# Optimization experiments

Hardware: AMD Instinct MI355X
Metric: run time of the kernel (lower is better)

Reference implementation:

```python
import jax, jax.numpy as jnp
import numpy as np

N, IN, HID, OUT, HEADS = 50000, 128, 128, 16, 4
EL, EG = 800000, 200000
NEG_SLOPE = 0.2


def setup_inputs() -> dict:
    key = jax.random.key(0)
    ks = jax.random.split(key, 24)
    def gn(k, shape, fan_in):
        return (jax.random.normal(k, shape, jnp.float32) / np.sqrt(fan_in)).astype(jnp.float32)
    inp = {}
    inp['x'] = jax.random.normal(ks[0], (N, IN), jnp.float32)
    inp['local_edge_index'] = jax.random.randint(ks[1], (2, EL), 0, N, jnp.int64 if jax.config.jax_enable_x64 else jnp.int32)
    inp['global_edge_index'] = jax.random.randint(ks[2], (2, EG), 0, N, jnp.int64 if jax.config.jax_enable_x64 else jnp.int32)
    # local_processor: Linear(IN, HID)
    inp['W1'] = gn(ks[3], (IN, HID), IN); inp['b1'] = jnp.zeros((HID,), jnp.float32)
    # GCNConv(HID, HID): weight + bias
    inp['Wg'] = gn(ks[4], (HID, HID), HID); inp['bg'] = jnp.zeros((HID,), jnp.float32)
    # GATConv(HID, HID, heads=4, concat=False): lin to HEADS*HID, att vectors, bias of size HID
    inp['Wa'] = gn(ks[5], (HID, HEADS * HID), HID)
    inp['att_src'] = gn(ks[6], (HEADS, HID), HID)
    inp['att_dst'] = gn(ks[7], (HEADS, HID), HID)
    inp['ba'] = jnp.zeros((HID,), jnp.float32)
    # hierarchical_pool: Linear(2*HID, HID)
    inp['Wp'] = gn(ks[8], (2 * HID, HID), 2 * HID); inp['bp'] = jnp.zeros((HID,), jnp.float32)
    # classifier: Linear(HID, HID//2) -> ReLU -> Linear(HID//2, OUT)
    inp['Wc1'] = gn(ks[9], (HID, HID // 2), HID); inp['bc1'] = jnp.zeros((HID // 2,), jnp.float32)
    inp['Wc2'] = gn(ks[10], (HID // 2, OUT), HID // 2); inp['bc2'] = jnp.zeros((OUT,), jnp.float32)
    # uncertainty_head: Linear(HID, OUT)
    inp['Wu'] = gn(ks[11], (HID, OUT), HID); inp['bu'] = jnp.zeros((OUT,), jnp.float32)
    return inp


def _add_self_loops(ei, n):
    loop = jnp.arange(n, dtype=ei.dtype)
    return jnp.concatenate([ei[0], loop]), jnp.concatenate([ei[1], loop])


def gcn_conv(x, ei, W, b):
    n = x.shape[0]
    xw = x @ W                                        # [N, HID]
    src, dst = _add_self_loops(ei, n)
    deg = jax.ops.segment_sum(jnp.ones_like(dst, dtype=xw.dtype), dst, num_segments=n)
    dinv = jax.lax.rsqrt(jnp.maximum(deg, 1e-12))     # deg >= 1 thanks to self-loops
    norm = dinv[src] * dinv[dst]                      # [E+N]
    msg = xw[src] * norm[:, None]                     # gather + scale
    return jax.ops.segment_sum(msg, dst, num_segments=n) + b


def gat_conv(x, ei, W, att_src, att_dst, b):
    n = x.shape[0]
    h, c = att_src.shape
    xw = (x @ W).reshape(n, h, c)                     # [N, H, C]
    a_s = jnp.einsum('nhc,hc->nh', xw, att_src)       # [N, H]
    a_d = jnp.einsum('nhc,hc->nh', xw, att_dst)
    src, dst = _add_self_loops(ei, n)
    e = jax.nn.leaky_relu(a_s[src] + a_d[dst], NEG_SLOPE)   # [E+N, H]
    emax = jax.ops.segment_max(e, dst, num_segments=n)      # stable edge-softmax per dst
    ee = jnp.exp(e - emax[dst])
    denom = jax.ops.segment_sum(ee, dst, num_segments=n)
    alpha = ee / (denom[dst] + 1e-16)                        # [E+N, H]
    out = jax.ops.segment_sum(xw[src] * alpha[:, :, None], dst, num_segments=n)  # [N,H,C]
    return out.mean(axis=1) + b                              # concat=False -> head mean


def reference(x, local_edge_index, global_edge_index, W1, b1, Wg, bg, Wa, att_src, att_dst, ba, Wp, bp, Wc1, bc1, Wc2, bc2, Wu, bu):
    x_local = jax.nn.relu(x @ W1 + b1)                       # dropout is identity in eval
    x_lg = jax.nn.relu(gcn_conv(x_local, local_edge_index, Wg, bg))
    x_gg = jax.nn.relu(gat_conv(x_local, global_edge_index, Wa, att_src, att_dst, ba))
    x_comb = jnp.concatenate([x_lg, x_gg], axis=1)           # [N, 2*HID]
    x_pooled = jax.nn.relu(x_comb @ Wp + bp)
    x_final = x_pooled.mean(axis=0, keepdims=True)           # batch=None path
    prediction = jax.nn.relu(x_final @ Wc1 + bc1) @ Wc2 + bc2
    uncertainty = jax.nn.sigmoid(x_final @ Wu + bu)
    return prediction, uncertainty
```

## Files before the change

kernel.cpp:

```cpp
#include <hip/hip_runtime.h>
#include <hip/hip_bf16.h>

#define N_NODES 50000
#define F_IN 128
#define HID 128
#define N_OUT 16
#define HEADS 4
#define EL 800000
#define EG 200000
#define NEG_SLOPE 0.2f
#define NB 196
#define GB 391

typedef short bf16x8 __attribute__((ext_vector_type(8)));
typedef float f32x4 __attribute__((ext_vector_type(4)));
typedef float f32x2 __attribute__((ext_vector_type(2)));

static __device__ __forceinline__ float lrelu(float x) {
    return x > 0.f ? x : NEG_SLOPE * x;
}
static __device__ __forceinline__ unsigned short f2b(float f) {
    __hip_bfloat16 h = __float2bfloat16(f);
    return *reinterpret_cast<unsigned short*>(&h);
}
static __device__ __forceinline__ unsigned char f2fp8(float f) {
    unsigned pk = __builtin_amdgcn_cvt_pk_fp8_f32(f, f, 0, false);
    return (unsigned char)(pk & 0xFF);
}
static __device__ __forceinline__ f32x2 fp8x2_to_f32(unsigned u) {
    return __builtin_amdgcn_cvt_pk_f32_fp8((int)u, false);
}

__global__ __launch_bounds__(256) void conv_hist(
    const float* __restrict__ W1, unsigned short* __restrict__ W1t,
    const float* __restrict__ Wg, unsigned short* __restrict__ Wgt,
    const float* __restrict__ Wa, unsigned short* __restrict__ Wat,
    const float* __restrict__ Wp, unsigned short* __restrict__ Wpt,
    const int* __restrict__ ldst, const int* __restrict__ gdst, int* __restrict__ ghist)
{
    int b = blockIdx.x, t = threadIdx.x;
    if (b < 64) {
        int idx = b * 256 + t;
        int k = idx >> 7, n = idx & 127;
        W1t[n * 128 + k] = f2b(W1[idx]);
    } else if (b < 128) {
        int idx = (b - 64) * 256 + t;
        int k = idx >> 7, n = idx & 127;
        Wgt[n * 128 + k] = f2b(Wg[idx]);
    } else if (b < 384) {
        int idx = (b - 128) * 256 + t;
        int k = idx >> 9, n = idx & 511;
        Wat[(size_t)n * 128 + k] = f2b(Wa[idx]);
    } else if (b < 512) {
        int idx = (b - 384) * 256 + t;
        int k = idx >> 7, n = idx & 127;
        Wpt[(size_t)n * 256 + k] = f2b(Wp[idx]);
    } else {
        __shared__ int lh[NB];
        int blk = b - 512;
        bool loc = blk < 196;
        const int* dstp = loc ? ldst : gdst;
        int nE = loc ? EL : EG;
        int* gh = ghist + (loc ? 0 : NB);
        int start = (loc ? blk : blk - 196) * 4096;
        if (t < NB) lh[t] = 0;
        __syncthreads();
        #pragma unroll
        for (int i = 0; i < 16; i++) {
            int e = start + i * 256 + t;
            if (e < nE) atomicAdd(&lh[dstp[e] >> 8], 1);
        }
        __syncthreads();
        if (t < NB && lh[t]) atomicAdd(&gh[t], lh[t]);
    }
}
__global__ void bucket_scan(const int* __restrict__ ghist,
                            int* __restrict__ bbase, int* __restrict__ gcur)
{
    __shared__ int s[256];
    int g = blockIdx.x, t = threadIdx.x;
    int v = (t < NB) ? ghist[g * NB + t] : 0;
    s[t] = v;
    __syncthreads();
    for (int off = 1; off < 256; off <<= 1) {
        int u = (t >= off) ? s[t - off] : 0;
        __syncthreads();
        s[t] += u;
        __syncthreads();
    }
    if (t < NB) {
        bbase[g * (NB + 1) + t] = s[t] - v;
        gcur[g * NB + t] = s[t] - v;
    }
    if (t == NB - 1) bbase[g * (NB + 1) + NB] = s[t];
}
__global__ __launch_bounds__(256) void bucket_part(
    const int* __restrict__ lsrc, const int* __restrict__ ldst,
    const int* __restrict__ gsrc, const int* __restrict__ gdst,
    int* __restrict__ gcur, unsigned* __restrict__ ebuf_l, unsigned* __restrict__ ebuf_g)
{
    __shared__ int lhist[NB], lbase[NB];
    int blk = blockIdx.x, t = threadIdx.x;
    bool loc = blk < 196;
    const int* srcp = loc ? lsrc : gsrc;
    const int* dstp = loc ? ldst : gdst;
    int nE = loc ? EL : EG;
    unsigned* ebuf = loc ? ebuf_l : ebuf_g;
    int* cur = gcur + (loc ? 0 : NB);
    int start = (loc ? blk : blk - 196) * 4096;
    if (t < NB) lhist[t] = 0;
    __syncthreads();
    unsigned pk[16];
    #pragma unroll
    for (int i = 0; i < 16; i++) {
        int e = start + i * 256 + t;
        if (e < nE) {
            unsigned d = (unsigned)dstp[e];
            pk[i] = (d << 16) | (unsigned)srcp[e];
            atomicAdd(&lhist[d >> 8], 1);
        } else pk[i] = 0xFFFFFFFFu;
    }
    __syncthreads();
    if (t < NB) lbase[t] = atomicAdd(&cur[t], lhist[t]);
    __syncthreads();
    if (t < NB) lhist[t] = 0;
    __syncthreads();
    #pragma unroll
    for (int i = 0; i < 16; i++) {
        unsigned b = pk[i] >> 24;
        if (b < NB) {
            int r = atomicAdd(&lhist[b], 1);
            ebuf[lbase[b] + r] = pk[i];
        }
    }
}
__global__ __launch_bounds__(256) void bucket_csr(
    const unsigned* __restrict__ ebuf_l, const unsigned* __restrict__ ebuf_g,
    const int* __restrict__ bbase,
    int* __restrict__ offs_l, int* __restrict__ offs_g,
    unsigned short* __restrict__ csr_l, unsigned short* __restrict__ csr_g,
    float* __restrict__ dinv)
{
    __shared__ int cnt[256], s[256], cur[256];
    int blk = blockIdx.x, t = threadIdx.x;
    bool loc = blk < 196;
    int b = loc ? blk : blk - 196;
    const unsigned* ebuf = loc ? ebuf_l : ebuf_g;
    const int* bb = bbase + (loc ? 0 : NB + 1);
    int* offs = loc ? offs_l : offs_g;
    unsigned short* csr = loc ? csr_l : csr_g;
    int rs = bb[b], re = bb[b + 1];
    cnt[t] = 0;
    __syncthreads();
    for (int i = rs + t; i < re; i += 256) atomicAdd(&cnt[(ebuf[i] >> 16) & 255], 1);
    __syncthreads();
    int v = cnt[t];
    s[t] = v;
    __syncthreads();
    for (int off = 1; off < 256; off <<= 1) {
        int u = (t >= off) ? s[t - off] : 0;
        __syncthreads();
        s[t] += u;
        __syncthreads();
    }
    int excl = s[t] - v;
    int node = b * 256 + t;
    cur[t] = rs + excl;
    if (node < N_NODES) {
        offs[node] = rs + excl;
        if (loc) dinv[node] = rsqrtf((float)(v + 1));
    }
    if (blk == 0 && t == 0) offs_l[N_NODES] = EL;
    if (blk == 196 && t == 0) offs_g[N_NODES] = EG;
    __syncthreads();
    for (int i = rs + t; i < re; i += 256) {
        unsigned pk = ebuf[i];
        int r = atomicAdd(&cur[(pk >> 16) & 255], 1);
        csr[r] = (unsigned short)(pk & 0xFFFFu);
    }
}

__global__ __launch_bounds__(256) void gemm_x(
    const float* __restrict__ A, const unsigned short* __restrict__ Bt,
    const float* __restrict__ bias, unsigned short* __restrict__ out, int M)
{
    __shared__ unsigned short As[128 * 128];
    __shared__ unsigned short Bs[128 * 128];
    int tid = threadIdx.x;
    int lane = tid & 63, w = tid >> 6;
    int wr = w >> 1, wc = w & 1;
    int l16 = lane & 15, lhi = lane >> 4;
    int m0 = blockIdx.x * 128;
    f32x4 acc[4][4] = {};
    #pragma unroll
    for (int i = 0; i < 8; i++) {
        int u = tid + i * 256;
        int row = u >> 4, e0 = (u & 15) << 3;
        int sw = e0 ^ ((row & 7) << 3);
        int gr = m0 + row;
        unsigned short pb[8] = {};
        if (gr < M) {
            float4 a0 = *(const float4*)(A + (size_t)gr * 128 + e0);
            float4 a1 = *(const float4*)(A + (size_t)gr * 128 + e0 + 4);
            pb[0] = f2b(a0.x); pb[1] = f2b(a0.y); pb[2] = f2b(a0.z); pb[3] = f2b(a0.w);
            pb[4] = f2b(a1.x); pb[5] = f2b(a1.y); pb[6] = f2b(a1.z); pb[7] = f2b(a1.w);
        }
        *(bf16x8*)(As + row * 128 + sw) = *(bf16x8*)pb;
        bf16x8 vb = *(const bf16x8*)(Bt + (size_t)row * 128 + e0);
        *(bf16x8*)(Bs + row * 128 + sw) = vb;
    }
    __syncthreads();
    #pragma unroll
    for (int kk = 0; kk < 4; kk++) {
        int ke = kk * 32 + lhi * 8;
        bf16x8 af[4], bfr[4];
        #pragma unroll
        for (int m = 0; m < 4; m++) {
            int r = wr * 64 + m * 16 + l16;
            af[m] = *(const bf16x8*)(As + r * 128 + (ke ^ ((r & 7) << 3)));
        }
        #pragma unroll
        for (int n = 0; n < 4; n++) {
            int r = wc * 64 + n * 16 + l16;
            bfr[n] = *(const bf16x8*)(Bs + r * 128 + (ke ^ ((r & 7) << 3)));
        }
        #pragma unroll
        for (int m = 0; m < 4; m++)
            #pragma unroll
            for (int n = 0; n < 4; n++)
                acc[m][n] = __builtin_amdgcn_mfma_f32_16x16x32_bf16(af[m], bfr[n], acc[m][n], 0, 0, 0);
    }
    #pragma unroll
    for (int m = 0; m < 4; m++) {
        #pragma unroll
        for (int r = 0; r < 4; r++) {
            int row_g = m0 + wr * 64 + m * 16 + lhi * 4 + r;
            if (row_g >= M) continue;
            #pragma unroll
            for (int n = 0; n < 4; n++) {
                int col_g = wc * 64 + n * 16 + l16;
                float v = fmaxf(acc[m][n][r] + bias[col_g], 0.f);
                out[(size_t)row_g * 128 + col_g] = f2b(v);
            }
        }
    }
}

__global__ __launch_bounds__(256) void gemm_gw(
    const unsigned short* __restrict__ A, const unsigned short* __restrict__ Wgt,
    const unsigned short* __restrict__ Wat,
    unsigned char* __restrict__ xw_g8, unsigned char* __restrict__ xw_a8, int M,
    const float* __restrict__ atts, const float* __restrict__ attd,
    float* __restrict__ a_s, float* __restrict__ a_d)
{
    __shared__ unsigned short As[128 * 128];
    __shared__ unsigned short Bs[128 * 128];
    __shared__ float sas[128], sad[128];
    int tid = threadIdx.x;
    int lane = tid & 63, w = tid >> 6;
    int wr = w >> 1, wc = w & 1;
    int l16 = lane & 15, lhi = lane >> 4;
    int m0 = blockIdx.x * 128;
    int hy = (int)blockIdx.y - 1;
    const unsigned short* Bt = (hy < 0) ? Wgt : (Wat + (size_t)hy * 128 * 128);
    f32x4 acc[4][4] = {};
    #pragma unroll
    for (int i = 0; i < 8; i++) {
        int u = tid + i * 256;
        int row = u >> 4, e0 = (u & 15) << 3;
        int sw = e0 ^ ((row & 7) << 3);
        bf16x8 va = {};
        int gr = m0 + row;
        if (gr < M) va = *(const bf16x8*)(A + (size_t)gr * 128 + e0);
        *(bf16x8*)(As + row * 128 + sw) = va;
        bf16x8 vb = *(const bf16x8*)(Bt + (size_t)row * 128 + e0);
        *(bf16x8*)(Bs + row * 128 + sw) = vb;
    }
    if (tid < 128) { sas[tid] = 0.f; sad[tid] = 0.f; }
    __syncthreads();
    #pragma unroll
    for (int kk = 0; kk < 4; kk++) {
        int ke = kk * 32 + lhi * 8;
        bf16x8 af[4], bfr[4];
        #pragma unroll
        for (int m = 0; m < 4; m++) {
            int r = wr * 64 + m * 16 + l16;
            af[m] = *(const bf16x8*)(As + r * 128 + (ke ^ ((r & 7) << 3)));
        }
        #pragma unroll
        for (int n = 0; n < 4; n++) {
            int r = wc * 64 + n * 16 + l16;
            bfr[n] = *(const bf16x8*)(Bs + r * 128 + (ke ^ ((r & 7) << 3)));
        }
        #pragma unroll
        for (int m = 0; m < 4; m++)
            #pragma unroll
            for (int n = 0; n < 4; n++)
                acc[m][n] = __builtin_amdgcn_mfma_f32_16x16x32_bf16(af[m], bfr[n], acc[m][n], 0, 0, 0);
    }
    if (hy < 0) {
        #pragma unroll
        for (int m = 0; m < 4; m++)
            #pragma unroll
            for (int r = 0; r < 4; r++) {
                int row_g = m0 + wr * 64 + m * 16 + lhi * 4 + r;
                if (row_g >= M) continue;
                #pragma unroll
                for (int n = 0; n < 4; n++) {
                    int col_g = wc * 64 + n * 16 + l16;
                    xw_g8[(size_t)row_g * 128 + col_g] = f2fp8(acc[m][n][r]);
                }
            }
    } else {
        float ats[4], atd[4];
        #pragma unroll
        for (int n = 0; n < 4; n++) {
            int cl = wc * 64 + n * 16 + l16;
            ats[n] = atts[hy * 128 + cl];
            atd[n] = attd[hy * 128 + cl];
        }
        #pragma unroll
        for (int m = 0; m < 4; m++) {
            #pragma unroll
            for (int r = 0; r < 4; r++) {
                int row_l = wr * 64 + m * 16 + lhi * 4 + r;
                int row_g = m0 + row_l;
                float ps = 0.f, pd = 0.f;
                #pragma unroll
                for (int n = 0; n < 4; n++) {
                    float v = acc[m][n][r];
                    ps = fmaf(v, ats[n], ps);
                    pd = fmaf(v, atd[n], pd);
                    if (row_g < M) {
                        int col_g = hy * 128 + wc * 64 + n * 16 + l16;
                        xw_a8[(size_t)row_g * 512 + col_g] = f2fp8(v);
                    }
                }
                #pragma unroll
                for (int off = 1; off < 16; off <<= 1) {
                    ps += __shfl_xor(ps, off);
                    pd += __shfl_xor(pd, off);
                }
                if (l16 == 0) {
                    atomicAdd(&sas[row_l], ps);
                    atomicAdd(&sad[row_l], pd);
                }
            }
        }
        __syncthreads();
        if (tid < 128) {
            int row_g = m0 + tid;
            if (row_g < M) {
                a_s[(size_t)row_g * 4 + hy] = sas[tid];
                a_d[(size_t)row_g * 4 + hy] = sad[tid];
            }
        }
    }
}

__global__ __launch_bounds__(256) void fused_gather(
    const int* __restrict__ offs_l, const unsigned short* __restrict__ csr_l,
    const unsigned char* __restrict__ xw_g8, const float* __restrict__ dinv,
    const float* __restrict__ bg,
    const int* __restrict__ offs_g, const unsigned short* __restrict__ csr_g,
    const float* __restrict__ a_s, const float* __restrict__ a_d,
    const unsigned char* __restrict__ xw_a8, const float* __restrict__ ba,
    unsigned short* __restrict__ xcomb)
{
    int blk = blockIdx.x;
    int lane = threadIdx.x & 63;
    int c2 = lane * 2;
    if (blk < 12500) {
        int d = (blk * 256 + threadIdx.x) >> 6;
        if (d >= N_NODES) return;
        const unsigned short* xg = (const unsigned short*)xw_g8;
        int base = offs_l[d], end = offs_l[d + 1];
        float ax = 0.f, ay = 0.f;
        for (int i = base; i < end; ) {
            int chunk = min(64, end - i);
            int sv = 0; float dvv = 0.f;
            if (lane < chunk) { sv = csr_l[i + lane]; dvv = dinv[sv]; }
            int j = 0;
            for (; j + 8 <= chunk; j += 8) {
                #pragma unroll
                for (int q = 0; q < 8; q++) {
                    int s = __shfl(sv, j + q);
                    float dv = __shfl(dvv, j + q);
                    f32x2 v = fp8x2_to_f32(xg[(size_t)s * 64 + lane]);
                    ax = fmaf(v[0], dv, ax);
                    ay = fmaf(v[1], dv, ay);
                }
            }
            for (; j < chunk; j++) {
                int s = __shfl(sv, j);
                float dv = __shfl(dvv, j);
                f32x2 v = fp8x2_to_f32(xg[(size_t)s * 64 + lane]);
                ax = fmaf(v[0], dv, ax);
                ay = fmaf(v[1], dv, ay);
            }
            i += chunk;
        }
        float dd = dinv[d];
        f32x2 sv2 = fp8x2_to_f32(xg[(size_t)d * 64 + lane]);
        float ox = fmaxf(dd * ax + dd * dd * sv2[0] + bg[c2], 0.f);
        float oy = fmaxf(dd * ay + dd * dd * sv2[1] + bg[c2 + 1], 0.f);
        unsigned uo = (unsigned)f2b(ox) | ((unsigned)f2b(oy) << 16);
        *(unsigned*)(xcomb + (size_t)d * 256 + c2) = uo;
    } else {
        int d = ((blk - 12500) * 256 + threadIdx.x) >> 6;
        if (d >= N_NODES) return;
        const unsigned short* xa = (const unsigned short*)xw_a8;
        int base = offs_g[d], end = offs_g[d + 1];
        int deg = end - base;
        float4 ad4 = *(const float4*)(a_d + (size_t)d * 4);
        float4 asd = *(const float4*)(a_s + (size_t)d * 4);
        float es0 = lrelu(asd.x + ad4.x), es1 = lrelu(asd.y + ad4.y);
        float es2 = lrelu(asd.z + ad4.z), es3 = lrelu(asd.w + ad4.w);
        float ax = 0.f, ay = 0.f;
        float m0, m1, m2, m3, r0, r1, r2, r3;
        if (deg <= 64) {
            int sv = 0;
            float e0 = -1e30f, e1 = -1e30f, e2 = -1e30f, e3 = -1e30f;
            if (lane < deg) {
                sv = csr_g[base + lane];
                float4 s4 = *(const float4*)(a_s + (size_t)sv * 4);
                e0 = lrelu(s4.x + ad4.x); e1 = lrelu(s4.y + ad4.y);
                e2 = lrelu(s4.z + ad4.z); e3 = lrelu(s4.w + ad4.w);
            }
            m0 = e0; m1 = e1; m2 = e2; m3 = e3;
            #pragma unroll
            for (int off = 1; off < 64; off <<= 1) {
                m0 = fmaxf(m0, __shfl_xor(m0, off));
                m1 = fmaxf(m1, __shfl_xor(m1, off));
                m2 = fmaxf(m2, __shfl_xor(m2, off));
                m3 = fmaxf(m3, __shfl_xor(m3, off));
            }
            m0 = fmaxf(m0, es0); m1 = fmaxf(m1, es1);
            m2 = fmaxf(m2, es2); m3 = fmaxf(m3, es3);
            float w0 = (lane < deg) ? __expf(e0 - m0) : 0.f;
            float w1 = (lane < deg) ? __expf(e1 - m1) : 0.f;
            float w2 = (lane < deg) ? __expf(e2 - m2) : 0.f;
            float w3 = (lane < deg) ? __expf(e3 - m3) : 0.f;
            float d0 = w0, d1 = w1, d2 = w2, d3 = w3;
            #pragma unroll
            for (int off = 1; off < 64; off <<= 1) {
                d0 += __shfl_xor(d0, off); d1 += __shfl_xor(d1, off);
                d2 += __shfl_xor(d2, off); d3 += __shfl_xor(d3, off);
            }
            d0 += __expf(es0 - m0); d1 += __expf(es1 - m1);
            d2 += __expf(es2 - m2); d3 += __expf(es3 - m3);
            r0 = 1.f / (d0 + 1e-16f); r1 = 1.f / (d1 + 1e-16f);
            r2 = 1.f / (d2 + 1e-16f); r3 = 1.f / (d3 + 1e-16f);
            for (int j = 0; j < deg; j++) {
                int s = __shfl(sv, j);
                float a0 = __shfl(w0, j) * r0, a1 = __shfl(w1, j) * r1;
                float a2 = __shfl(w2, j) * r2, a3 = __shfl(w3, j) * r3;
                const unsigned short* row = xa + (size_t)s * 256 + lane;
                f32x2 v0 = fp8x2_to_f32(row[0]);
                f32x2 v1 = fp8x2_to_f32(row[64]);
                f32x2 v2 = fp8x2_to_f32(row[128]);
                f32x2 v3 = fp8x2_to_f32(row[192]);
                ax = fmaf(v0[0], a0, ax); ay = fmaf(v0[1], a0, ay);
                ax = fmaf(v1[0], a1, ax); ay = fmaf(v1[1], a1, ay);
                ax = fmaf(v2[0], a2, ax); ay = fmaf(v2[1], a2, ay);
                ax = fmaf(v3[0], a3, ax); ay = fmaf(v3[1], a3, ay);
            }
        } else {
            m0 = es0; m1 = es1; m2 = es2; m3 = es3;
            for (int i = base; i < end; i += 64) {
                int c = min(64, end - i);
                float t0 = -1e30f, t1 = -1e30f, t2 = -1e30f, t3 = -1e30f;
                if (lane < c) {
                    int s = csr_g[i + lane];
                    float4 s4 = *(const float4*)(a_s + (size_t)s * 4);
                    t0 = lrelu(s4.x + ad4.x); t1 = lrelu(s4.y + ad4.y);
                    t2 = lrelu(s4.z + ad4.z); t3 = lrelu(s4.w + ad4.w);
                }
                m0 = fmaxf(m0, t0); m1 = fmaxf(m1, t1);
                m2 = fmaxf(m2, t2); m3 = fmaxf(m3, t3);
            }
            #pragma unroll
            for (int off = 1; off < 64; off <<= 1) {
                m0 = fmaxf(m0, __shfl_xor(m0, off));
                m1 = fmaxf(m1, __shfl_xor(m1, off));
                m2 = fmaxf(m2, __shfl_xor(m2, off));
                m3 = fmaxf(m3, __shfl_xor(m3, off));
            }
            float d0 = 0.f, d1 = 0.f, d2 = 0.f, d3 = 0.f;
            for (int i = base; i < end; i += 64) {
                int c = min(64, end - i);
                if (lane < c) {
                    int s = csr_g[i + lane];
                    float4 s4 = *(const float4*)(a_s + (size_t)s * 4);
                    d0 += __expf(lrelu(s4.x + ad4.x) - m0);
                    d1 += __expf(lrelu(s4.y + ad4.y) - m1);
                    d2 += __expf(lrelu(s4.z + ad4.z) - m2);
                    d3 += __expf(lrelu(s4.w + ad4.w) - m3);
                }
            }
            #pragma unroll
            for (int off = 1; off < 64; off <<= 1) {
                d0 += __shfl_xor(d0, off); d1 += __shfl_xor(d1, off);
                d2 += __shfl_xor(d2, off); d3 += __shfl_xor(d3, off);
            }
            d0 += __expf(es0 - m0); d1 += __expf(es1 - m1);
            d2 += __expf(es2 - m2); d3 += __expf(es3 - m3);
            r0 = 1.f / (d0 + 1e-16f); r1 = 1.f / (d1 + 1e-16f);
            r2 = 1.f / (d2 + 1e-16f); r3 = 1.f / (d3 + 1e-16f);
            for (int i = base; i < end; i += 64) {
                int c = min(64, end - i);
                int sv = 0;
                float w0 = 0.f, w1 = 0.f, w2 = 0.f, w3 = 0.f;
                if (lane < c) {
                    sv = csr_g[i + lane];
                    float4 s4 = *(const float4*)(a_s + (size_t)sv * 4);
                    w0 = __expf(lrelu(s4.x + ad4.x) - m0) * r0;
                    w1 = __expf(lrelu(s4.y + ad4.y) - m1) * r1;
                    w2 = __expf(lrelu(s4.z + ad4.z) - m2) * r2;
                    w3 = __expf(lrelu(s4.w + ad4.w) - m3) * r3;
                }
                for (int j = 0; j < c; j++) {
                    int s = __shfl(sv, j);
                    float a0 = __shfl(w0, j), a1 = __shfl(w1, j);
                    float a2 = __shfl(w2, j), a3 = __shfl(w3, j);
                    const unsigned short* row = xa + (size_t)s * 256 + lane;
                    f32x2 v0 = fp8x2_to_f32(row[0]);
                    f32x2 v1 = fp8x2_to_f32(row[64]);
                    f32x2 v2 = fp8x2_to_f32(row[128]);
                    f32x2 v3 = fp8x2_to_f32(row[192]);
                    ax = fmaf(v0[0], a0, ax); ay = fmaf(v0[1], a0, ay);
                    ax = fmaf(v1[0], a1, ax); ay = fmaf(v1[1], a1, ay);
                    ax = fmaf(v2[0], a2, ax); ay = fmaf(v2[1], a2, ay);
                    ax = fmaf(v3[0], a3, ax); ay = fmaf(v3[1], a3, ay);
                }
            }
        }
        float s0 = __expf(es0 - m0) * r0, s1 = __expf(es1 - m1) * r1;
        float s2 = __expf(es2 - m2) * r2, s3 = __expf(es3 - m3) * r3;
        const unsigned short* row = xa + (size_t)d * 256 + lane;
        f32x2 v0 = fp8x2_to_f32(row[0]);
        f32x2 v1 = fp8x2_to_f32(row[64]);
        f32x2 v2 = fp8x2_to_f32(row[128]);
        f32x2 v3 = fp8x2_to_f32(row[192]);
        ax = fmaf(v0[0], s0, ax); ay = fmaf(v0[1], s0, ay);
        ax = fmaf(v1[0], s1, ax); ay = fmaf(v1[1], s1, ay);
        ax = fmaf(v2[0], s2, ax); ay = fmaf(v2[1], s2, ay);
        ax = fmaf(v3[0], s3, ax); ay = fmaf(v3[1], s3, ay);
        float ox = fmaxf(0.25f * ax + ba[c2], 0.f);
        float oy = fmaxf(0.25f * ay + ba[c2 + 1], 0.f);
        unsigned uo = (unsigned)f2b(ox) | ((unsigned)f2b(oy) << 16);
        *(unsigned*)(xcomb + (size_t)d * 256 + 128 + c2) = uo;
    }
}

__global__ __launch_bounds__(256) void mfma_pool(
    const unsigned short* __restrict__ A, const unsigned short* __restrict__ Bt,
    const float* __restrict__ bp, float* __restrict__ sumvec, int M)
{
    __shared__ unsigned short As[128 * 128];
    __shared__ unsigned short Bs[128 * 128];
    __shared__ float red[128];
    int tid = threadIdx.x;
    int lane = tid & 63, w = tid >> 6;
    int wr = w >> 1, wc = w & 1;
    int l16 = lane & 15, lhi = lane >> 4;
    int m0 = blockIdx.x * 128;
    f32x4 acc[4][4] = {};
    for (int kb = 0; kb < 256; kb += 128) {
        if (kb) __syncthreads();
        #pragma unroll
        for (int i = 0; i < 8; i++) {
            int u = tid + i * 256;
            int row = u >> 4, e0 = (u & 15) << 3;
            int sw = e0 ^ ((row & 7) << 3);
            bf16x8 va = {};
            int gr = m0 + row;
            if (gr < M) va = *(const bf16x8*)(A + (size_t)gr * 256 + kb + e0);
            *(bf16x8*)(As + row * 128 + sw) = va;
            bf16x8 vb = *(const bf16x8*)(Bt + (size_t)row * 256 + kb + e0);
            *(bf16x8*)(Bs + row * 128 + sw) = vb;
        }
        __syncthreads();
        #pragma unroll
        for (int kk = 0; kk < 4; kk++) {
            int ke = kk * 32 + lhi * 8;
            bf16x8 af[4], bfr[4];
            #pragma unroll
            for (int m = 0; m < 4; m++) {
                int r = wr * 64 + m * 16 + l16;
                af[m] = *(const bf16x8*)(As + r * 128 + (ke ^ ((r & 7) << 3)));
            }
            #pragma unroll
            for (int n = 0; n < 4; n++) {
                int r = wc * 64 + n * 16 + l16;
                bfr[n] = *(const bf16x8*)(Bs + r * 128 + (ke ^ ((r & 7) << 3)));
            }
            #pragma unroll
            for (int m = 0; m < 4; m++)
                #pragma unroll
                for (int n = 0; n < 4; n++)
                    acc[m][n] = __builtin_amdgcn_mfma_f32_16x16x32_bf16(af[m], bfr[n], acc[m][n], 0, 0, 0);
        }
    }
    float bcol[4];
    #pragma unroll
    for (int n = 0; n < 4; n++) bcol[n] = bp[wc * 64 + n * 16 + l16];
    float colsum[4] = {0.f, 0.f, 0.f, 0.f};
    #pragma unroll
    for (int m = 0; m < 4; m++) {
        #pragma unroll
        for (int r = 0; r < 4; r++) {
            int row_g = m0 + wr * 64 + m * 16 + lhi * 4 + r;
            if (row_g < M) {
                #pragma unroll
                for (int n = 0; n < 4; n++)
                    colsum[n] += fmaxf(acc[m][n][r] + bcol[n], 0.f);
            }
        }
    }
    #pragma unroll
    for (int n = 0; n < 4; n++) {
        colsum[n] += __shfl_xor(colsum[n], 16);
        colsum[n] += __shfl_xor(colsum[n], 32);
    }
    if (tid < 128) red[tid] = 0.f;
    __syncthreads();
    if (lhi == 0) {
        #pragma unroll
        for (int n = 0; n < 4; n++)
            atomicAdd(&red[wc * 64 + n * 16 + l16], colsum[n]);
    }
    __syncthreads();
    if (tid < 128) atomicAdd(&sumvec[tid], red[tid]);
}

__global__ void final_head(const float* __restrict__ sumvec,
                           const float* __restrict__ Wc1, const float* __restrict__ bc1,
                           const float* __restrict__ Wc2, const float* __restrict__ bc2,
                           const float* __restrict__ Wu, const float* __restrict__ bu,
                           float* __restrict__ out)
{
    __shared__ float xf[128];
    __shared__ float h1[64];
    int t = threadIdx.x;
    xf[t] = sumvec[t] * (1.0f / N_NODES);
    __syncthreads();
    if (t < 64) {
        float s = bc1[t];
        for (int c = 0; c < 128; c++) s = fmaf(xf[c], Wc1[c * 64 + t], s);
        h1[t] = fmaxf(s, 0.f);
    }
    __syncthreads();
    if (t < 16) {
        float s = bc2[t];
        for (int j = 0; j < 64; j++) s = fmaf(h1[j], Wc2[j * 16 + t], s);
        out[t] = s;
        float u = bu[t];
        for (int c = 0; c < 128; c++) u = fmaf(xf[c], Wu[c * 16 + t], u);
        out[16 + t] = 1.0f / (1.0f + expf(-u));
    }
}

extern "C" void kernel_launch(void* const* d_in, const int* in_sizes, int n_in,
                              void* d_out, int out_size, void* d_ws, size_t ws_size,
                              hipStream_t stream) {
    const float* x    = (const float*)d_in[0];
    const int*   lei  = (const int*)d_in[1];
    const int*   gei  = (const int*)d_in[2];
    const float* W1   = (const float*)d_in[3];
    const float* b1   = (const float*)d_in[4];
    const float* Wg   = (const float*)d_in[5];
    const float* bg   = (const float*)d_in[6];
    const float* Wa   = (const float*)d_in[7];
    const float* atts = (const float*)d_in[8];
    const float* attd = (const float*)d_in[9];
    const float* ba   = (const float*)d_in[10];
    const float* Wp   = (const float*)d_in[11];
    const float* bp   = (const float*)d_in[12];
    const float* Wc1  = (const float*)d_in[13];
    const float* bc1  = (const float*)d_in[14];
    const float* Wc2  = (const float*)d_in[15];
    const float* bc2  = (const float*)d_in[16];
    const float* Wu   = (const float*)d_in[17];
    const float* bu   = (const float*)d_in[18];

    const int* lsrc = lei;
    const int* ldst = lei + EL;
    const int* gsrc = gei;
    const int* gdst = gei + EG;

    uintptr_t base = (uintptr_t)d_ws;
    auto alloc = [&](size_t bytes) { void* p = (void*)base; base += (bytes + 255) & ~(size_t)255; return p; };
    unsigned short* x_loc  = (unsigned short*)alloc((size_t)N_NODES * 128 * 2);
    unsigned char*  xw_g8  = (unsigned char*)alloc((size_t)N_NODES * 128);
    unsigned char*  xw_a8  = (unsigned char*)alloc((size_t)N_NODES * 512);
    unsigned short* xcomb  = (unsigned short*)alloc((size_t)N_NODES * 256 * 2);
    unsigned short* W1t    = (unsigned short*)alloc((size_t)128 * 128 * 2);
    unsigned short* Wgt    = (unsigned short*)alloc((size_t)128 * 128 * 2);
    unsigned short* Wat    = (unsigned short*)alloc((size_t)512 * 128 * 2);
    unsigned short* Wpt    = (unsigned short*)alloc((size_t)128 * 256 * 2);
    float* dinv       = (float*)alloc((size_t)N_NODES * 4);
    float* a_s        = (float*)alloc((size_t)N_NODES * 4 * 4);
    float* a_d        = (float*)alloc((size_t)N_NODES * 4 * 4);
    int*   ghist      = (int*)alloc((size_t)2 * NB * 4);
    int*   bbase      = (int*)alloc((size_t)2 * (NB + 1) * 4);
    int*   gcur       = (int*)alloc((size_t)2 * NB * 4);
    unsigned* ebuf_l  = (unsigned*)alloc((size_t)EL * 4);
    unsigned* ebuf_g  = (unsigned*)alloc((size_t)EG * 4);
    int*   offs_l     = (int*)alloc(((size_t)N_NODES + 1) * 4);
    int*   offs_g     = (int*)alloc(((size_t)N_NODES + 1) * 4);
    unsigned short* csr_l = (unsigned short*)alloc((size_t)EL * 2);
    unsigned short* csr_g = (unsigned short*)alloc((size_t)EG * 2);
    float* sumvec     = (float*)alloc(128 * 4);

    hipMemsetAsync(ghist, 0, (size_t)2 * NB * 4, stream);
    hipMemsetAsync(sumvec, 0, 128 * 4, stream);

    conv_hist<<<757, 256, 0, stream>>>(W1, W1t, Wg, Wgt, Wa, Wat, Wp, Wpt,
                                       ldst, gdst, ghist);
    bucket_scan<<<2, 256, 0, stream>>>(ghist, bbase, gcur);
    bucket_part<<<245, 256, 0, stream>>>(lsrc, ldst, gsrc, gdst, gcur, ebuf_l, ebuf_g);
    bucket_csr<<<392, 256, 0, stream>>>(ebuf_l, ebuf_g, bbase, offs_l, offs_g,
                                        csr_l, csr_g, dinv);

    gemm_x<<<GB, 256, 0, stream>>>(x, W1t, b1, x_loc, N_NODES);

    gemm_gw<<<dim3(GB, 5), 256, 0, stream>>>(x_loc, Wgt, Wat, xw_g8, xw_a8, N_NODES,
                                             atts, attd, a_s, a_d);

    fused_gather<<<25000, 256, 0, stream>>>(offs_l, csr_l, xw_g8, dinv, bg,
                                            offs_g, csr_g, a_s, a_d, xw_a8, ba, xcomb);

    mfma_pool<<<GB, 256, 0, stream>>>(xcomb, Wpt, bp, sumvec, N_NODES);
    final_head<<<1, 128, 0, stream>>>(sumvec, Wc1, bc1, Wc2, bc2, Wu, bu,
                                      (float*)d_out);
}
```

Before: 193.6 us.

## Restructure gather to wide 8-byte loads with sub-wave edge parallelism

The GCN gather now splits each wavefront into four 16-lane groups. Each group handles a different edge and loads 8 fp8 values per lane, and the groups' partial sums are combined with cross-group shuffles at the end. The GAT small-degree path maps each 16-lane group to one head, broadcasts source indices and weights with readlane, and applies the softmax normalization once per edge. The aim is fewer, wider memory transactions and fewer shuffle instructions per edge, at the cost of extra reduction shuffles and idle lanes during the final store.

```diff
diff --git a/kernel.cpp b/kernel.cpp
--- a/kernel.cpp
+++ b/kernel.cpp
@@ -29,6 +29,9 @@
 }
 static __device__ __forceinline__ f32x2 fp8x2_to_f32(unsigned u) {
     return __builtin_amdgcn_cvt_pk_f32_fp8((int)u, false);
+}
+static __device__ __forceinline__ float rdlane_f(float v, int l) {
+    return __int_as_float(__builtin_amdgcn_readlane(__float_as_int(v), l));
 }
 
 __global__ __launch_bounds__(256) void conv_hist(
@@ -369,55 +372,69 @@
 {
     int blk = blockIdx.x;
     int lane = threadIdx.x & 63;
-    int c2 = lane * 2;
+    int g = lane >> 4, q = lane & 15;
     if (blk < 12500) {
         int d = (blk * 256 + threadIdx.x) >> 6;
         if (d >= N_NODES) return;
-        const unsigned short* xg = (const unsigned short*)xw_g8;
         int base = offs_l[d], end = offs_l[d + 1];
-        float ax = 0.f, ay = 0.f;
+        float acc[8] = {};
         for (int i = base; i < end; ) {
             int chunk = min(64, end - i);
             int sv = 0; float dvv = 0.f;
             if (lane < chunk) { sv = csr_l[i + lane]; dvv = dinv[sv]; }
-            int j = 0;
-            for (; j + 8 <= chunk; j += 8) {
-                #pragma unroll
-                for (int q = 0; q < 8; q++) {
-                    int s = __shfl(sv, j + q);
-                    float dv = __shfl(dvv, j + q);
-                    f32x2 v = fp8x2_to_f32(xg[(size_t)s * 64 + lane]);
-                    ax = fmaf(v[0], dv, ax);
-                    ay = fmaf(v[1], dv, ay);
-                }
-            }
-            for (; j < chunk; j++) {
-                int s = __shfl(sv, j);
-                float dv = __shfl(dvv, j);
-                f32x2 v = fp8x2_to_f32(xg[(size_t)s * 64 + lane]);
-                ax = fmaf(v[0], dv, ax);
-                ay = fmaf(v[1], dv, ay);
+            int nst = (chunk + 3) >> 2;
+            for (int j = 0; j < nst; j++) {
+                int e = j * 4 + g;
+                int s = __shfl(sv, e);
+                float dv = __shfl(dvv, e);
+                if (e >= chunk) dv = 0.f;
+                uint2 v = *(const uint2*)(xw_g8 + (size_t)s * 128 + q * 8);
+                f32x2 p0 = __builtin_amdgcn_cvt_pk_f32_fp8((int)v.x, false);
+                f32x2 p1 = __builtin_amdgcn_cvt_pk_f32_fp8((int)v.x, true);
+                f32x2 p2 = __builtin_amdgcn_cvt_pk_f32_fp8((int)v.y, false);
+                f32x2 p3 = __builtin_amdgcn_cvt_pk_f32_fp8((int)v.y, true);
+                acc[0] = fmaf(p0[0], dv, acc[0]); acc[1] = fmaf(p0[1], dv, acc[1]);
+                acc[2] = fmaf(p1[0], dv, acc[2]); acc[3] = fmaf(p1[1], dv, acc[3]);
+                acc[4] = fmaf(p2[0], dv, acc[4]); acc[5] = fmaf(p2[1], dv, acc[5]);
+                acc[6] = fmaf(p3[0], dv, acc[6]); acc[7] = fmaf(p3[1], dv, acc[7]);
             }
             i += chunk;
         }
-        float dd = dinv[d];
-        f32x2 sv2 = fp8x2_to_f32(xg[(size_t)d * 64 + lane]);
-        float ox = fmaxf(dd * ax + dd * dd * sv2[0] + bg[c2], 0.f);
-        float oy = fmaxf(dd * ay + dd * dd * sv2[1] + bg[c2 + 1], 0.f);
-        unsigned uo = (unsigned)f2b(ox) | ((unsigned)f2b(oy) << 16);
-        *(unsigned*)(xcomb + (size_t)d * 256 + c2) = uo;
+        #pragma unroll
+        for (int k = 0; k < 8; k++) {
+            acc[k] += __shfl_xor(acc[k], 16);
+            acc[k] += __shfl_xor(acc[k], 32);
+        }
+        if (g == 0) {
+            float dd = dinv[d];
+            float d2 = dd * dd;
+            uint2 sv2 = *(const uint2*)(xw_g8 + (size_t)d * 128 + q * 8);
+            f32x2 s0 = __builtin_amdgcn_cvt_pk_f32_fp8((int)sv2.x, false);
+            f32x2 s1 = __builtin_amdgcn_cvt_pk_f32_fp8((int)sv2.x, true);
+            f32x2 s2 = __builtin_amdgcn_cvt_pk_f32_fp8((int)sv2.y, false);
+            f32x2 s3 = __builtin_amdgcn_cvt_pk_f32_fp8((int)sv2.y, true);
+            float sf[8] = {s0[0], s0[1], s1[0], s1[1], s2[0], s2[1], s3[0], s3[1]};
+            float4 b0 = *(const float4*)(bg + q * 8);
+            float4 b1 = *(const float4*)(bg + q * 8 + 4);
+            float bb[8] = {b0.x, b0.y, b0.z, b0.w, b1.x, b1.y, b1.z, b1.w};
+            unsigned o[4];
+            #pragma unroll
+            for (int k = 0; k < 4; k++) {
+                float v0 = fmaxf(dd * acc[2 * k] + d2 * sf[2 * k] + bb[2 * k], 0.f);
+                float v1 = fmaxf(dd * acc[2 * k + 1] + d2 * sf[2 * k + 1] + bb[2 * k + 1], 0.f);
+                o[k] = (unsigned)f2b(v0) | ((unsigned)f2b(v1) << 16);
+            }
+            *(uint4*)(xcomb + (size_t)d * 256 + q * 8) = make_uint4(o[0], o[1], o[2], o[3]);
+        }
     } else {
         int d = ((blk - 12500) * 256 + threadIdx.x) >> 6;
         if (d >= N_NODES) return;
-        const unsigned short* xa = (const unsigned short*)xw_a8;
         int base = offs_g[d], end = offs_g[d + 1];
         int deg = end - base;
         float4 ad4 = *(const float4*)(a_d + (size_t)d * 4);
         float4 asd = *(const float4*)(a_s + (size_t)d * 4);
         float es0 = lrelu(asd.x + ad4.x), es1 = lrelu(asd.y + ad4.y);
         float es2 = lrelu(asd.z + ad4.z), es3 = lrelu(asd.w + ad4.w);
-        float ax = 0.f, ay = 0.f;
-        float m0, m1, m2, m3, r0, r1, r2, r3;
         if (deg <= 64) {
             int sv = 0;
             float e0 = -1e30f, e1 = -1e30f, e2 = -1e30f, e3 = -1e30f;
@@ -427,7 +444,7 @@
                 e0 = lrelu(s4.x + ad4.x); e1 = lrelu(s4.y + ad4.y);
                 e2 = lrelu(s4.z + ad4.z); e3 = lrelu(s4.w + ad4.w);
             }
-            m0 = e0; m1 = e1; m2 = e2; m3 = e3;
+            float m0 = e0, m1 = e1, m2 = e2, m3 = e3;
             #pragma unroll
             for (int off = 1; off < 64; off <<= 1) {
                 m0 = fmaxf(m0, __shfl_xor(m0, off));
@@ -449,24 +466,62 @@
             }
             d0 += __expf(es0 - m0); d1 += __expf(es1 - m1);
             d2 += __expf(es2 - m2); d3 += __expf(es3 - m3);
-            r0 = 1.f / (d0 + 1e-16f); r1 = 1.f / (d1 + 1e-16f);
-            r2 = 1.f / (d2 + 1e-16f); r3 = 1.f / (d3 + 1e-16f);
+            float r0 = 1.f / (d0 + 1e-16f), r1 = 1.f / (d1 + 1e-16f);
+            float r2 = 1.f / (d2 + 1e-16f), r3 = 1.f / (d3 + 1e-16f);
+            w0 *= r0; w1 *= r1; w2 *= r2; w3 *= r3;
+            float acc[8] = {};
+            const unsigned char* xa = xw_a8;
+            int goff = g * 128 + q * 8;
             for (int j = 0; j < deg; j++) {
-                int s = __shfl(sv, j);
-                float a0 = __shfl(w0, j) * r0, a1 = __shfl(w1, j) * r1;
-                float a2 = __shfl(w2, j) * r2, a3 = __shfl(w3, j) * r3;
-                const unsigned short* row = xa + (size_t)s * 256 + lane;
-                f32x2 v0 = fp8x2_to_f32(row[0]);
-                f32x2 v1 = fp8x2_to_f32(row[64]);
-                f32x2 v2 = fp8x2_to_f32(row[128]);
-                f32x2 v3 = fp8x2_to_f32(row[192]);
-                ax = fmaf(v0[0], a0, ax); ay = fmaf(v0[1], a0, ay);
-                ax = fmaf(v1[0], a1, ax); ay = fmaf(v1[1], a1, ay);
-                ax = fmaf(v2[0], a2, ax); ay = fmaf(v2[1], a2, ay);
-                ax = fmaf(v3[0], a3, ax); ay = fmaf(v3[1], a3, ay);
+                int s = __builtin_amdgcn_readlane(sv, j);
+                float a0 = rdlane_f(w0, j), a1 = rdlane_f(w1, j);
+                float a2 = rdlane_f(w2, j), a3 = rdlane_f(w3, j);
+                float al = (g == 0) ? a0 : (g == 1) ? a1 : (g == 2) ? a2 : a3;
+                uint2 v = *(const uint2*)(xa + (size_t)s * 512 + goff);
+                f32x2 p0 = __builtin_amdgcn_cvt_pk_f32_fp8((int)v.x, false);
+                f32x2 p1 = __builtin_amdgcn_cvt_pk_f32_fp8((int)v.x, true);
+                f32x2 p2 = __builtin_amdgcn_cvt_pk_f32_fp8((int)v.y, false);
+                f32x2 p3 = __builtin_amdgcn_cvt_pk_f32_fp8((int)v.y, true);
+                acc[0] = fmaf(p0[0], al, acc[0]); acc[1] = fmaf(p0[1], al, acc[1]);
+                acc[2] = fmaf(p1[0], al, acc[2]); acc[3] = fmaf(p1[1], al, acc[3]);
+                acc[4] = fmaf(p2[0], al, acc[4]); acc[5] = fmaf(p2[1], al, acc[5]);
+                acc[6] = fmaf(p3[0], al, acc[6]); acc[7] = fmaf(p3[1], al, acc[7]);
+            }
+            float es_s = (g == 0) ? es0 : (g == 1) ? es1 : (g == 2) ? es2 : es3;
+            float m_s  = (g == 0) ? m0  : (g == 1) ? m1  : (g == 2) ? m2  : m3;
+            float r_s  = (g == 0) ? r0  : (g == 1) ? r1  : (g == 2) ? r2  : r3;
+            float s_al = __expf(es_s - m_s) * r_s;
+            uint2 v = *(const uint2*)(xa + (size_t)d * 512 + goff);
+            f32x2 p0 = __builtin_amdgcn_cvt_pk_f32_fp8((int)v.x, false);
+            f32x2 p1 = __builtin_amdgcn_cvt_pk_f32_fp8((int)v.x, true);
+            f32x2 p2 = __builtin_amdgcn_cvt_pk_f32_fp8((int)v.y, false);
+            f32x2 p3 = __builtin_amdgcn_cvt_pk_f32_fp8((int)v.y, true);
+            acc[0] = fmaf(p0[0], s_al, acc[0]); acc[1] = fmaf(p0[1], s_al, acc[1]);
+            acc[2] = fmaf(p1[0], s_al, acc[2]); acc[3] = fmaf(p1[1], s_al, acc[3]);
+            acc[4] = fmaf(p2[0], s_al, acc[4]); acc[5] = fmaf(p2[1], s_al, acc[5]);
+            acc[6] = fmaf(p3[0], s_al, acc[6]); acc[7] = fmaf(p3[1], s_al, acc[7]);
+            #pragma unroll
+            for (int k = 0; k < 8; k++) {
+                acc[k] += __shfl_xor(acc[k], 16);
+                acc[k] += __shfl_xor(acc[k], 32);
+            }
+            if (g == 0) {
+                float4 b0 = *(const float4*)(ba + q * 8);
+                float4 b1 = *(const float4*)(ba + q * 8 + 4);
+                float bb[8] = {b0.x, b0.y, b0.z, b0.w, b1.x, b1.y, b1.z, b1.w};
+                unsigned o[4];
+                #pragma unroll
+                for (int k = 0; k < 4; k++) {
+                    float v0 = fmaxf(0.25f * acc[2 * k] + bb[2 * k], 0.f);
+                    float v1 = fmaxf(0.25f * acc[2 * k + 1] + bb[2 * k + 1], 0.f);
+                    o[k] = (unsigned)f2b(v0) | ((unsigned)f2b(v1) << 16);
+                }
+                *(uint4*)(xcomb + (size_t)d * 256 + 128 + q * 8) = make_uint4(o[0], o[1], o[2], o[3]);
             }
         } else {
-            m0 = es0; m1 = es1; m2 = es2; m3 = es3;
+            int c2 = lane * 2;
+            const unsigned short* xa = (const unsigned short*)xw_a8;
+            float m0 = es0, m1 = es1, m2 = es2, m3 = es3;
             for (int i = base; i < end; i += 64) {
                 int c = min(64, end - i);
                 float t0 = -1e30f, t1 = -1e30f, t2 = -1e30f, t3 = -1e30f;
@@ -505,8 +560,9 @@
             }
             d0 += __expf(es0 - m0); d1 += __expf(es1 - m1);
             d2 += __expf(es2 - m2); d3 += __expf(es3 - m3);
-            r0 = 1.f / (d0 + 1e-16f); r1 = 1.f / (d1 + 1e-16f);
-            r2 = 1.f / (d2 + 1e-16f); r3 = 1.f / (d3 + 1e-16f);
+            float r0 = 1.f / (d0 + 1e-16f), r1 = 1.f / (d1 + 1e-16f);
+            float r2 = 1.f / (d2 + 1e-16f), r3 = 1.f / (d3 + 1e-16f);
+            float ax = 0.f, ay = 0.f;
             for (int i = base; i < end; i += 64) {
                 int c = min(64, end - i);
                 int sv = 0;
@@ -534,22 +590,22 @@
                     ax = fmaf(v3[0], a3, ax); ay = fmaf(v3[1], a3, ay);
                 }
             }
-        }
-        float s0 = __expf(es0 - m0) * r0, s1 = __expf(es1 - m1) * r1;
-        float s2 = __expf(es2 - m2) * r2, s3 = __expf(es3 - m3) * r3;
-        const unsigned short* row = xa + (size_t)d * 256 + lane;
-        f32x2 v0 = fp8x2_to_f32(row[0]);
-        f32x2 v1 = fp8x2_to_f32(row[64]);
-        f32x2 v2 = fp8x2_to_f32(row[128]);
-        f32x2 v3 = fp8x2_to_f32(row[192]);
-        ax = fmaf(v0[0], s0, ax); ay = fmaf(v0[1], s0, ay);
-        ax = fmaf(v1[0], s1, ax); ay = fmaf(v1[1], s1, ay);
-        ax = fmaf(v2[0], s2, ax); ay = fmaf(v2[1], s2, ay);
-        ax = fmaf(v3[0], s3, ax); ay = fmaf(v3[1], s3, ay);
-        float ox = fmaxf(0.25f * ax + ba[c2], 0.f);
-        float oy = fmaxf(0.25f * ay + ba[c2 + 1], 0.f);
-        unsigned uo = (unsigned)f2b(ox) | ((unsigned)f2b(oy) << 16);
-        *(unsigned*)(xcomb + (size_t)d * 256 + 128 + c2) = uo;
+            float s0 = __expf(es0 - m0) * r0, s1 = __expf(es1 - m1) * r1;
+            float s2 = __expf(es2 - m2) * r2, s3 = __expf(es3 - m3) * r3;
+            const unsigned short* row = xa + (size_t)d * 256 + lane;
+            f32x2 v0 = fp8x2_to_f32(row[0]);
+            f32x2 v1 = fp8x2_to_f32(row[64]);
+            f32x2 v2 = fp8x2_to_f32(row[128]);
+            f32x2 v3 = fp8x2_to_f32(row[192]);
+            ax = fmaf(v0[0], s0, ax); ay = fmaf(v0[1], s0, ay);
+            ax = fmaf(v1[0], s1, ax); ay = fmaf(v1[1], s1, ay);
+            ax = fmaf(v2[0], s2, ax); ay = fmaf(v2[1], s2, ay);
+            ax = fmaf(v3[0], s3, ax); ay = fmaf(v3[1], s3, ay);
+            float ox = fmaxf(0.25f * ax + ba[c2], 0.f);
+            float oy = fmaxf(0.25f * ay + ba[c2 + 1], 0.f);
+            unsigned uo = (unsigned)f2b(ox) | ((unsigned)f2b(oy) << 16);
+            *(unsigned*)(xcomb + (size_t)d * 256 + 128 + c2) = uo;
+        }
     }
 }
 
@@ -724,7 +780,6 @@
                                         csr_l, csr_g, dinv);
 
     gemm_x<<<GB, 256, 0, stream>>>(x, W1t, b1, x_loc, N_NODES);
-
     gemm_gw<<<dim3(GB, 5), 256, 0, stream>>>(x_loc, Wgt, Wat, xw_g8, xw_a8, N_NODES,
                                              atts, attd, a_s, a_d);
 
```

After: 195.1 us. About the same (+0.8%).
